# Kernel tuning notes

Hardware: AMD Instinct MI355X
Metric: run time of the kernel (lower is better)

## Reference

```python
import jax, jax.numpy as jnp
import numpy as np

N_NODES = 50000
N_EDGES = 800000


def _sage_conv(x, src, dst, Wl, Wr, b):
    # PyG SAGEConv (aggr='mean', root_weight=True):
    #   out_i = lin_l(mean_{j->i} x_j) + lin_r(x_i)
    msg = x[src]                                             # [E, F] gather
    agg = jax.ops.segment_sum(msg, dst, num_segments=N_NODES)
    deg = jax.ops.segment_sum(jnp.ones((msg.shape[0],), x.dtype), dst,
                              num_segments=N_NODES)
    agg = agg / jnp.maximum(deg, 1.0)[:, None]               # mean aggregation
    return agg @ Wl + x @ Wr + b


def setup_inputs() -> dict:
    key = jax.random.key(0)
    ks = jax.random.split(key, 9)
    Fin, H1, H2, Fout = 128, 256, 128, 64

    def w(k, fi, fo):
        return jax.random.normal(k, (fi, fo), jnp.float32) / np.sqrt(fi)

    return {
        "x": jax.random.normal(ks[0], (N_NODES, Fin), jnp.float32),
        "edge_index": jax.random.randint(ks[1], (2, N_EDGES), 0, N_NODES,
                                         dtype=jnp.int64),
        "Wl1": w(ks[2], Fin, H1), "Wr1": w(ks[3], Fin, H1),
        "b1": jnp.zeros((H1,), jnp.float32),
        "Wl2": w(ks[4], H1, H2), "Wr2": w(ks[5], H1, H2),
        "b2": jnp.zeros((H2,), jnp.float32),
        "Wl3": w(ks[6], H2, Fout), "Wr3": w(ks[7], H2, Fout),
        "b3": jnp.zeros((Fout,), jnp.float32),
    }


def reference(x, edge_index, Wl1, Wr1, b1, Wl2, Wr2, b2, Wl3, Wr3, b3):
    src, dst = edge_index[0], edge_index[1]
    # conv1 -> ReLU -> (dropout: identity in eval) -> conv2 -> ReLU -> conv3 -> Sigmoid
    h = jax.nn.relu(_sage_conv(x, src, dst, Wl1, Wr1, b1))
    h = jax.nn.relu(_sage_conv(h, src, dst, Wl2, Wr2, b2))
    out = jax.nn.sigmoid(_sage_conv(h, src, dst, Wl3, Wr3, b3))
    return out
```

## Files before the change

kernel.cpp:

```cpp
#include <hip/hip_runtime.h>
#include <cstddef>


using frag  = __attribute__((ext_vector_type(8))) short;
using f32x4 = __attribute__((ext_vector_type(4))) float;

constexpr int PBITS = 9;
constexpr int PSZ   = 1 << PBITS;
constexpr int PMAX  = 128;

__device__ __forceinline__ ushort f2bf(float f) {
    union { float f; unsigned u; } v; v.f = f;
    unsigned r = v.u + 0x7FFF + ((v.u >> 16) & 1);
    return (ushort)(r >> 16);
}
__device__ __forceinline__ float bf2f(ushort u) {
    union { unsigned u; float f; } v; v.u = ((unsigned)u) << 16;
    return v.f;
}


__global__ __launch_bounds__(256)
void k_pcount(const int* __restrict__ dst, int* __restrict__ pcount, int E, int P) {
    __shared__ int h[PMAX];
    int t = threadIdx.x;
    if (t < P) h[t] = 0;
    __syncthreads();
    int base = blockIdx.x * 4096;
    int n = min(4096, E - base);
    for (int i = t; i < n; i += 256)
        atomicAdd(&h[dst[base + i] >> PBITS], 1);
    __syncthreads();
    if (t < P && h[t]) atomicAdd(&pcount[t], h[t]);
}

__global__ void k_pscan(const int* __restrict__ pcount, int* __restrict__ pbase,
                        int* __restrict__ pcursor, int P) {
    if (threadIdx.x == 0) {
        int run = 0;
        for (int p = 0; p < P; ++p) { pbase[p] = run; pcursor[p] = run; run += pcount[p]; }
        pbase[P] = run;
    }
}

__global__ __launch_bounds__(256)
void k_scatter(const int* __restrict__ src, const int* __restrict__ dst,
               int* __restrict__ pcursor, unsigned* __restrict__ pairs, int E, int P) {
    __shared__ int h[PMAX];
    __shared__ int off[PMAX];
    int t = threadIdx.x;
    if (t < P) h[t] = 0;
    __syncthreads();
    int base = blockIdx.x * 4096;
    int pp[16]; int pr[16]; unsigned pk[16];
    #pragma unroll
    for (int ii = 0; ii < 16; ++ii) {
        int idx = base + ii * 256 + t;
        bool v = idx < E;
        int d = v ? dst[idx] : 0;
        int p = d >> PBITS;
        pp[ii] = v ? p : -1;
        pr[ii] = v ? atomicAdd(&h[p], 1) : 0;
        pk[ii] = v ? ((unsigned)src[idx] | ((unsigned)(d & (PSZ - 1)) << 16)) : 0u;
    }
    __syncthreads();
    if (t < P && h[t]) off[t] = atomicAdd(&pcursor[t], h[t]);
    __syncthreads();
    #pragma unroll
    for (int ii = 0; ii < 16; ++ii)
        if (pp[ii] >= 0) pairs[off[pp[ii]] + pr[ii]] = pk[ii];
}

__global__ __launch_bounds__(256)
void k_build(const unsigned* __restrict__ pairs, const int* __restrict__ pbase,
             int* __restrict__ deg, int* __restrict__ row_start,
             ushort* __restrict__ csr16, int M) {
    __shared__ int cnt[PSZ];
    __shared__ int ls[PSZ];
    __shared__ int fil[PSZ];
    __shared__ int ws[256];
    int pid = blockIdx.x;
    int t = threadIdx.x;
    int n0 = pid << PBITS;
    int L = min(PSZ, M - n0);
    int wb = pbase[pid], we = pbase[pid + 1];
    int ne = we - wb;
    for (int j = t; j < PSZ; j += 256) { cnt[j] = 0; fil[j] = 0; }
    __syncthreads();
    for (int i = t; i < ne; i += 256)
        atomicAdd(&cnt[pairs[wb + i] >> 16], 1);
    __syncthreads();
    int a = cnt[2 * t], b = cnt[2 * t + 1];
    ws[t] = a + b;
    __syncthreads();
    for (int o = 1; o < 256; o <<= 1) {
        int v = (t >= o) ? ws[t - o] : 0;
        __syncthreads();
        ws[t] += v;
        __syncthreads();
    }
    int excl = (t > 0) ? ws[t - 1] : 0;
    ls[2 * t] = excl; ls[2 * t + 1] = excl + a;
    __syncthreads();
    for (int j = t; j < L; j += 256) {
        deg[n0 + j] = cnt[j];
        row_start[n0 + j] = wb + ls[j];
    }
    for (int i = t; i < ne; i += 256) {
        unsigned pk = pairs[wb + i];
        int ln = pk >> 16;
        int pos = wb + ls[ln] + atomicAdd(&fil[ln], 1);
        csr16[pos] = (ushort)(pk & 0xFFFFu);
    }
}


__global__ void k_cvt_x(const float* __restrict__ in, ushort* __restrict__ out, int n4) {
    int i = blockIdx.x * blockDim.x + threadIdx.x;
    if (i < n4) {
        float4 v = ((const float4*)in)[i];
        ushort4 o; o.x = f2bf(v.x); o.y = f2bf(v.y); o.z = f2bf(v.z); o.w = f2bf(v.w);
        ((ushort4*)out)[i] = o;
    }
}

struct CvtDesc {
    const float* s[6];
    ushort*      d[6];
    int K[6];
    int N[6];
};

__global__ void k_cvt_w6(CvtDesc c) {
    int wi = blockIdx.y;
    int t = blockIdx.x * blockDim.x + threadIdx.x;
    int K = c.K[wi], N = c.N[wi];
    if (t < K * N) {
        int k = t / N, n = t % N;
        c.d[wi][(size_t)n * K + k] = f2bf(c.s[wi][t]);
    }
}


template <int F, int EPI>
__global__ __launch_bounds__(256)
void agg_bf(const ushort* __restrict__ in, const ushort* __restrict__ csr16,
            const int* __restrict__ row_start, const int* __restrict__ deg,
            const ushort* __restrict__ u, const float* __restrict__ bias,
            void* __restrict__ out, int nN) {
    constexpr int GPL = F / 4;
    constexpr int NPB = 256 / GPL;
    int gid  = threadIdx.x / GPL;
    int li   = threadIdx.x % GPL;
    int node = blockIdx.x * NPB + gid;
    bool valid = node < nN;
    int start = valid ? row_start[node] : 0;
    int d     = valid ? deg[node] : 0;
    float a0 = 0.f, a1 = 0.f, a2 = 0.f, a3 = 0.f;

    auto gat = [&](int j) {
        int s = csr16[start + j];
        ushort4 uv = *(const ushort4*)(in + (size_t)s * F + li * 4);
        a0 += bf2f(uv.x); a1 += bf2f(uv.y); a2 += bf2f(uv.z); a3 += bf2f(uv.w);
    };

    int j = 0;
    for (; j + 8 <= d; j += 8) {
        gat(j); gat(j+1); gat(j+2); gat(j+3);
        gat(j+4); gat(j+5); gat(j+6); gat(j+7);
    }
    for (; j + 2 <= d; j += 2) { gat(j); gat(j+1); }
    for (; j < d; ++j) gat(j);

    if (!valid) return;
    float inv = 1.f / (float)(d > 0 ? d : 1);
    a0 *= inv; a1 *= inv; a2 *= inv; a3 *= inv;

    size_t o4 = (size_t)node * F + li * 4;
    if constexpr (EPI == 0) {
        ushort4 o; o.x = f2bf(a0); o.y = f2bf(a1); o.z = f2bf(a2); o.w = f2bf(a3);
        *(ushort4*)((ushort*)out + o4) = o;
    } else {
        ushort4 uv = *(const ushort4*)(u + o4);
        float4 bv = *(const float4*)(bias + li * 4);
        a0 += bf2f(uv.x) + bv.x;
        a1 += bf2f(uv.y) + bv.y;
        a2 += bf2f(uv.z) + bv.z;
        a3 += bf2f(uv.w) + bv.w;
        if constexpr (EPI == 1) {
            ushort4 o;
            o.x = f2bf(fmaxf(a0, 0.f)); o.y = f2bf(fmaxf(a1, 0.f));
            o.z = f2bf(fmaxf(a2, 0.f)); o.w = f2bf(fmaxf(a3, 0.f));
            *(ushort4*)((ushort*)out + o4) = o;
        } else {
            float4 o;
            o.x = 1.f / (1.f + __expf(-a0)); o.y = 1.f / (1.f + __expf(-a1));
            o.z = 1.f / (1.f + __expf(-a2)); o.w = 1.f / (1.f + __expf(-a3));
            *(float4*)((float*)out + o4) = o;
        }
    }
}


__device__ __forceinline__ void gload16(const ushort* gp, char* lp) {
    __builtin_amdgcn_global_load_lds(
        (const __attribute__((address_space(1))) void*)gp,
        (__attribute__((address_space(3))) void*)lp, 16, 0, 0);
}

template <int BM, int BN, int WM, int WN, int ACT>
__global__ __launch_bounds__(WM * WN * 64)
void mgemm(const ushort* __restrict__ A1, const ushort* __restrict__ B1, int K1,
           const ushort* __restrict__ A2, const ushort* __restrict__ B2, int K2,
           const float* __restrict__ bias,
           ushort* __restrict__ C1, int ld1,
           ushort* __restrict__ C2, int ld2, int nsplit,
           int M, int N) {
    constexpr int NW = WM * WN;
    constexpr int MF = BM / (WM * 16);
    constexpr int NF = BN / (WN * 16);
    __shared__ char lds[(BM + BN) * 128];
    char* As = lds;
    char* Bs = lds + BM * 128;

    const int tid  = threadIdx.x;
    const int lane = tid & 63;
    const int wid  = tid >> 6;
    const int wm   = wid % WM, wn = wid / WM;
    const int bm   = blockIdx.x * BM;
    const int bn   = blockIdx.y * BN;
    const int l15  = lane & 15;
    const int lhi  = lane >> 4;
    const int lr8  = lane >> 3;
    const int lf   = lane & 7;

    f32x4 acc[MF][NF] = {};

    for (int pass = 0; pass < 2; ++pass) {
        const ushort* A = pass ? A2 : A1;
        const ushort* B = pass ? B2 : B1;
        const int K = pass ? K2 : K1;
        if (A == nullptr) continue;
        for (int k0 = 0; k0 < K; k0 += 64) {
            #pragma unroll
            for (int it = 0; it < BM / (8 * NW); ++it) {
                int r0 = (it * NW + wid) * 8;
                int row = r0 + lr8;
                int gr = bm + row; if (gr >= M) gr = M - 1;
                int gfc = lf ^ (row & 7);
                gload16(A + (size_t)gr * K + k0 + gfc * 8, As + r0 * 128);
            }
            #pragma unroll
            for (int it = 0; it < BN / (8 * NW); ++it) {
                int r0 = (it * NW + wid) * 8;
                int row = r0 + lr8;
                int gfc = lf ^ (row & 7);
                gload16(B + (size_t)(bn + row) * K + k0 + gfc * 8, Bs + r0 * 128);
            }
            __syncthreads();
            #pragma unroll
            for (int ks = 0; ks < 2; ++ks) {
                const int kb = ks * 64 + lhi * 16;
                frag a[MF], b[NF];
                #pragma unroll
                for (int mf = 0; mf < MF; ++mf) {
                    int row = wm * MF * 16 + mf * 16 + l15;
                    a[mf] = *(const frag*)(As + row * 128 + (kb ^ ((row & 7) << 4)));
                }
                #pragma unroll
                for (int nf = 0; nf < NF; ++nf) {
                    int row = wn * NF * 16 + nf * 16 + l15;
                    b[nf] = *(const frag*)(Bs + row * 128 + (kb ^ ((row & 7) << 4)));
                }
                #pragma unroll
                for (int mf = 0; mf < MF; ++mf)
                    #pragma unroll
                    for (int nf = 0; nf < NF; ++nf)
                        acc[mf][nf] = __builtin_amdgcn_mfma_f32_16x16x32_bf16(
                            a[mf], b[nf], acc[mf][nf], 0, 0, 0);
            }
            __syncthreads();
        }
    }

    #pragma unroll
    for (int mf = 0; mf < MF; ++mf) {
        #pragma unroll
        for (int r = 0; r < 4; ++r) {
            int gm = bm + wm * MF * 16 + mf * 16 + lhi * 4 + r;
            if (gm >= M) continue;
            #pragma unroll
            for (int nf = 0; nf < NF; ++nf) {
                int gn = bn + wn * NF * 16 + nf * 16 + l15;
                float v = acc[mf][nf][r];
                if (bias) v += bias[gn];
                if (ACT == 1) v = fmaxf(v, 0.f);
                ushort o = f2bf(v);
                if (gn < nsplit) C1[(size_t)gm * ld1 + gn] = o;
                else             C2[(size_t)gm * ld2 + (gn - nsplit)] = o;
            }
        }
    }
}


extern "C" void kernel_launch(void* const* d_in, const int* in_sizes, int n_in,
                              void* d_out, int out_size, void* d_ws, size_t ws_size,
                              hipStream_t stream) {
    const float* x   = (const float*)d_in[0];
    const int*   ei  = (const int*)d_in[1];
    const float* Wl1 = (const float*)d_in[2];
    const float* Wr1 = (const float*)d_in[3];
    const float* b1  = (const float*)d_in[4];
    const float* Wl2 = (const float*)d_in[5];
    const float* Wr2 = (const float*)d_in[6];
    const float* b2  = (const float*)d_in[7];
    const float* Wl3 = (const float*)d_in[8];
    const float* Wr3 = (const float*)d_in[9];
    const float* b3  = (const float*)d_in[10];

    const int M = in_sizes[0] / 128;
    const int E = in_sizes[1] / 2;
    const int P = (M + PSZ - 1) / PSZ;
    const int* src = ei;
    const int* dst = ei + E;

    char* w = (char*)d_ws;
    auto alloc = [&](size_t bytes) -> void* {
        void* p = (void*)w;
        w += (bytes + 255) & ~(size_t)255;
        return p;
    };
    int* pcount    = (int*)alloc((size_t)PMAX * 4);
    int* pbase     = (int*)alloc((size_t)(PMAX + 1) * 4);
    int* pcursor   = (int*)alloc((size_t)PMAX * 4);
    unsigned* pairs = (unsigned*)alloc((size_t)E * 4);
    ushort* csr16  = (ushort*)alloc((size_t)E * 2);
    int* deg       = (int*)alloc((size_t)M * 4);
    int* row_start = (int*)alloc((size_t)M * 4);
    ushort* Wl1t   = (ushort*)alloc(256 * 128 * 2);
    ushort* Wr1t   = (ushort*)alloc(256 * 128 * 2);
    ushort* Wcat2T = (ushort*)alloc(256 * 256 * 2);
    ushort* Wcat3T = (ushort*)alloc(128 * 128 * 2);
    ushort* bufA = (ushort*)alloc((size_t)M * 128 * 2);
    ushort* bufB = (ushort*)alloc((size_t)M * 128 * 2);
    ushort* bufH = (ushort*)alloc((size_t)M * 256 * 2);
    ushort* bufC = (ushort*)alloc((size_t)M * 128 * 2);
    (void)ws_size; (void)n_in; (void)out_size;

    ushort* x_bf = bufA; ushort* t2 = bufA; ushort* t3 = bufA;
    ushort* aggx = bufB; ushort* h2 = bufB;
    ushort* h1 = bufH;
    ushort* u2 = bufC;   ushort* u3 = bufC;

    hipMemsetAsync(pcount, 0, (size_t)PMAX * 4, stream);
    const int nchunk = (E + 4095) / 4096;
    k_pcount<<<nchunk, 256, 0, stream>>>(dst, pcount, E, P);
    k_pscan<<<1, 64, 0, stream>>>(pcount, pbase, pcursor, P);
    k_scatter<<<nchunk, 256, 0, stream>>>(src, dst, pcursor, pairs, E, P);
    k_build<<<P, 256, 0, stream>>>(pairs, pbase, deg, row_start, csr16, M);

    k_cvt_x<<<(M * 128 / 4 + 255) / 256, 256, 0, stream>>>(x, x_bf, M * 128 / 4);
    CvtDesc cd;
    cd.s[0] = Wl1; cd.d[0] = Wl1t;             cd.K[0] = 128; cd.N[0] = 256;
    cd.s[1] = Wr1; cd.d[1] = Wr1t;             cd.K[1] = 128; cd.N[1] = 256;
    cd.s[2] = Wl2; cd.d[2] = Wcat2T;           cd.K[2] = 256; cd.N[2] = 128;
    cd.s[3] = Wr2; cd.d[3] = Wcat2T + 128*256; cd.K[3] = 256; cd.N[3] = 128;
    cd.s[4] = Wl3; cd.d[4] = Wcat3T;           cd.K[4] = 128; cd.N[4] = 64;
    cd.s[5] = Wr3; cd.d[5] = Wcat3T + 64*128;  cd.K[5] = 128; cd.N[5] = 64;
    k_cvt_w6<<<dim3(128, 6), 256, 0, stream>>>(cd);

    const int gm128 = (M + 127) / 128;
    const int ga128 = (M + 7) / 8;
    const int ga64  = (M + 15) / 16;

    agg_bf<128, 0><<<ga128, 256, 0, stream>>>(x_bf, csr16, row_start, deg,
                                              nullptr, nullptr, aggx, M);
    mgemm<128, 64, 2, 2, 1><<<dim3(gm128, 4), 256, 0, stream>>>(
        aggx, Wl1t, 128, x_bf, Wr1t, 128, b1,
        h1, 256, nullptr, 0, 256, M, 256);

    mgemm<128, 64, 2, 2, 0><<<dim3(gm128, 4), 256, 0, stream>>>(
        h1, Wcat2T, 256, nullptr, nullptr, 0, nullptr,
        t2, 128, u2, 128, 128, M, 256);
    agg_bf<128, 1><<<ga128, 256, 0, stream>>>(t2, csr16, row_start, deg,
                                              u2, b2, h2, M);

    mgemm<128, 64, 2, 2, 0><<<dim3(gm128, 2), 256, 0, stream>>>(
        h2, Wcat3T, 128, nullptr, nullptr, 0, nullptr,
        t3, 64, u3, 64, 64, M, 128);
    agg_bf<64, 2><<<ga64, 256, 0, stream>>>(t3, csr16, row_start, deg,
                                            u3, b3, (float*)d_out, M);
}
```

Before: 215.7 us.

## Concatenate layer-1 operands, double-buffer GEMM LDS tiles, shrink GEMM tile to 64 rows

```diff
diff --git a/kernel.cpp b/kernel.cpp
--- a/kernel.cpp
+++ b/kernel.cpp
@@ -115,12 +115,14 @@
 }
 
 
-__global__ void k_cvt_x(const float* __restrict__ in, ushort* __restrict__ out, int n4) {
+__global__ void k_cvt_x(const float* __restrict__ in, ushort* __restrict__ AX, int n4) {
     int i = blockIdx.x * blockDim.x + threadIdx.x;
     if (i < n4) {
+        int row = i >> 5;
+        int c4  = i & 31;
         float4 v = ((const float4*)in)[i];
         ushort4 o; o.x = f2bf(v.x); o.y = f2bf(v.y); o.z = f2bf(v.z); o.w = f2bf(v.w);
-        ((ushort4*)out)[i] = o;
+        *(ushort4*)(AX + (size_t)row * 256 + 128 + c4 * 4) = o;
     }
 }
 
@@ -129,6 +131,8 @@
     ushort*      d[6];
     int K[6];
     int N[6];
+    int KD[6];
+    int KO[6];
 };
 
 __global__ void k_cvt_w6(CvtDesc c) {
@@ -137,12 +141,12 @@
     int K = c.K[wi], N = c.N[wi];
     if (t < K * N) {
         int k = t / N, n = t % N;
-        c.d[wi][(size_t)n * K + k] = f2bf(c.s[wi][t]);
-    }
-}
-
-
-template <int F, int EPI>
+        c.d[wi][(size_t)n * c.KD[wi] + c.KO[wi] + k] = f2bf(c.s[wi][t]);
+    }
+}
+
+
+template <int F, int EPI, int LDI, int LDO>
 __global__ __launch_bounds__(256)
 void agg_bf(const ushort* __restrict__ in, const ushort* __restrict__ csr16,
             const int* __restrict__ row_start, const int* __restrict__ deg,
@@ -160,7 +164,7 @@
 
     auto gat = [&](int j) {
         int s = csr16[start + j];
-        ushort4 uv = *(const ushort4*)(in + (size_t)s * F + li * 4);
+        ushort4 uv = *(const ushort4*)(in + (size_t)s * LDI + li * 4);
         a0 += bf2f(uv.x); a1 += bf2f(uv.y); a2 += bf2f(uv.z); a3 += bf2f(uv.w);
     };
 
@@ -176,12 +180,12 @@
     float inv = 1.f / (float)(d > 0 ? d : 1);
     a0 *= inv; a1 *= inv; a2 *= inv; a3 *= inv;
 
-    size_t o4 = (size_t)node * F + li * 4;
+    size_t o4 = (size_t)node * LDO + li * 4;
     if constexpr (EPI == 0) {
         ushort4 o; o.x = f2bf(a0); o.y = f2bf(a1); o.z = f2bf(a2); o.w = f2bf(a3);
         *(ushort4*)((ushort*)out + o4) = o;
     } else {
-        ushort4 uv = *(const ushort4*)(u + o4);
+        ushort4 uv = *(const ushort4*)(u + (size_t)node * F + li * 4);
         float4 bv = *(const float4*)(bias + li * 4);
         a0 += bf2f(uv.x) + bv.x;
         a1 += bf2f(uv.y) + bv.y;
@@ -208,20 +212,20 @@
         (__attribute__((address_space(3))) void*)lp, 16, 0, 0);
 }
 
-template <int BM, int BN, int WM, int WN, int ACT>
-__global__ __launch_bounds__(WM * WN * 64)
-void mgemm(const ushort* __restrict__ A1, const ushort* __restrict__ B1, int K1,
-           const ushort* __restrict__ A2, const ushort* __restrict__ B2, int K2,
+template <int BM, int BN, int K, int ACT>
+__global__ __launch_bounds__(256)
+void mgemm(const ushort* __restrict__ A, const ushort* __restrict__ B,
            const float* __restrict__ bias,
            ushort* __restrict__ C1, int ld1,
            ushort* __restrict__ C2, int ld2, int nsplit,
            int M, int N) {
-    constexpr int NW = WM * WN;
+    constexpr int NW = 4;
+    constexpr int WM = 2, WN = 2;
     constexpr int MF = BM / (WM * 16);
     constexpr int NF = BN / (WN * 16);
-    __shared__ char lds[(BM + BN) * 128];
-    char* As = lds;
-    char* Bs = lds + BM * 128;
+    constexpr int NSTEP = K / 64;
+    constexpr int TB = (BM + BN) * 128;
+    __shared__ char lds[2 * TB];
 
     const int tid  = threadIdx.x;
     const int lane = tid & 63;
@@ -234,52 +238,55 @@
     const int lr8  = lane >> 3;
     const int lf   = lane & 7;
 
+    auto stage = [&](int buf, int k0) {
+        char* As = lds + buf * TB;
+        char* Bs = As + BM * 128;
+        #pragma unroll
+        for (int it = 0; it < BM / (8 * NW); ++it) {
+            int r0 = (it * NW + wid) * 8;
+            int row = r0 + lr8;
+            int gr = bm + row; if (gr >= M) gr = M - 1;
+            int gfc = lf ^ (row & 7);
+            gload16(A + (size_t)gr * K + k0 + gfc * 8, As + r0 * 128);
+        }
+        #pragma unroll
+        for (int it = 0; it < BN / (8 * NW); ++it) {
+            int r0 = (it * NW + wid) * 8;
+            int row = r0 + lr8;
+            int gfc = lf ^ (row & 7);
+            gload16(B + (size_t)(bn + row) * K + k0 + gfc * 8, Bs + r0 * 128);
+        }
+    };
+
     f32x4 acc[MF][NF] = {};
 
-    for (int pass = 0; pass < 2; ++pass) {
-        const ushort* A = pass ? A2 : A1;
-        const ushort* B = pass ? B2 : B1;
-        const int K = pass ? K2 : K1;
-        if (A == nullptr) continue;
-        for (int k0 = 0; k0 < K; k0 += 64) {
+    stage(0, 0);
+    #pragma unroll
+    for (int s = 0; s < NSTEP; ++s) {
+        __syncthreads();
+        if (s + 1 < NSTEP) stage((s + 1) & 1, (s + 1) * 64);
+        char* As = lds + (s & 1) * TB;
+        char* Bs = As + BM * 128;
+        #pragma unroll
+        for (int ks = 0; ks < 2; ++ks) {
+            const int kb = ks * 64 + lhi * 16;
+            frag a[MF], b[NF];
             #pragma unroll
-            for (int it = 0; it < BM / (8 * NW); ++it) {
-                int r0 = (it * NW + wid) * 8;
-                int row = r0 + lr8;
-                int gr = bm + row; if (gr >= M) gr = M - 1;
-                int gfc = lf ^ (row & 7);
-                gload16(A + (size_t)gr * K + k0 + gfc * 8, As + r0 * 128);
+            for (int mf = 0; mf < MF; ++mf) {
+                int row = wm * MF * 16 + mf * 16 + l15;
+                a[mf] = *(const frag*)(As + row * 128 + (kb ^ ((row & 7) << 4)));
             }
             #pragma unroll
-            for (int it = 0; it < BN / (8 * NW); ++it) {
-                int r0 = (it * NW + wid) * 8;
-                int row = r0 + lr8;
-                int gfc = lf ^ (row & 7);
-                gload16(B + (size_t)(bn + row) * K + k0 + gfc * 8, Bs + r0 * 128);
+            for (int nf = 0; nf < NF; ++nf) {
+                int row = wn * NF * 16 + nf * 16 + l15;
+                b[nf] = *(const frag*)(Bs + row * 128 + (kb ^ ((row & 7) << 4)));
             }
-            __syncthreads();
             #pragma unroll
-            for (int ks = 0; ks < 2; ++ks) {
-                const int kb = ks * 64 + lhi * 16;
-                frag a[MF], b[NF];
+            for (int mf = 0; mf < MF; ++mf)
                 #pragma unroll
-                for (int mf = 0; mf < MF; ++mf) {
-                    int row = wm * MF * 16 + mf * 16 + l15;
-                    a[mf] = *(const frag*)(As + row * 128 + (kb ^ ((row & 7) << 4)));
-                }
-                #pragma unroll
-                for (int nf = 0; nf < NF; ++nf) {
-                    int row = wn * NF * 16 + nf * 16 + l15;
-                    b[nf] = *(const frag*)(Bs + row * 128 + (kb ^ ((row & 7) << 4)));
-                }
-                #pragma unroll
-                for (int mf = 0; mf < MF; ++mf)
-                    #pragma unroll
-                    for (int nf = 0; nf < NF; ++nf)
-                        acc[mf][nf] = __builtin_amdgcn_mfma_f32_16x16x32_bf16(
-                            a[mf], b[nf], acc[mf][nf], 0, 0, 0);
-            }
-            __syncthreads();
+                for (int nf = 0; nf < NF; ++nf)
+                    acc[mf][nf] = __builtin_amdgcn_mfma_f32_16x16x32_bf16(
+                        a[mf], b[nf], acc[mf][nf], 0, 0, 0);
         }
     }
 
@@ -338,18 +345,18 @@
     ushort* csr16  = (ushort*)alloc((size_t)E * 2);
     int* deg       = (int*)alloc((size_t)M * 4);
     int* row_start = (int*)alloc((size_t)M * 4);
-    ushort* Wl1t   = (ushort*)alloc(256 * 128 * 2);
-    ushort* Wr1t   = (ushort*)alloc(256 * 128 * 2);
+    ushort* Wcat1T = (ushort*)alloc(256 * 256 * 2);
     ushort* Wcat2T = (ushort*)alloc(256 * 256 * 2);
     ushort* Wcat3T = (ushort*)alloc(128 * 128 * 2);
+    ushort* AX   = (ushort*)alloc((size_t)M * 256 * 2);
     ushort* bufA = (ushort*)alloc((size_t)M * 128 * 2);
     ushort* bufB = (ushort*)alloc((size_t)M * 128 * 2);
     ushort* bufH = (ushort*)alloc((size_t)M * 256 * 2);
     ushort* bufC = (ushort*)alloc((size_t)M * 128 * 2);
     (void)ws_size; (void)n_in; (void)out_size;
 
-    ushort* x_bf = bufA; ushort* t2 = bufA; ushort* t3 = bufA;
-    ushort* aggx = bufB; ushort* h2 = bufB;
+    ushort* t2 = bufA; ushort* t3 = bufA;
+    ushort* h2 = bufB;
     ushort* h1 = bufH;
     ushort* u2 = bufC;   ushort* u3 = bufC;
 
@@ -360,35 +367,32 @@
     k_scatter<<<nchunk, 256, 0, stream>>>(src, dst, pcursor, pairs, E, P);
     k_build<<<P, 256, 0, stream>>>(pairs, pbase, deg, row_start, csr16, M);
 
-    k_cvt_x<<<(M * 128 / 4 + 255) / 256, 256, 0, stream>>>(x, x_bf, M * 128 / 4);
+    k_cvt_x<<<(M * 128 / 4 + 255) / 256, 256, 0, stream>>>(x, AX, M * 128 / 4);
     CvtDesc cd;
-    cd.s[0] = Wl1; cd.d[0] = Wl1t;             cd.K[0] = 128; cd.N[0] = 256;
-    cd.s[1] = Wr1; cd.d[1] = Wr1t;             cd.K[1] = 128; cd.N[1] = 256;
-    cd.s[2] = Wl2; cd.d[2] = Wcat2T;           cd.K[2] = 256; cd.N[2] = 128;
-    cd.s[3] = Wr2; cd.d[3] = Wcat2T + 128*256; cd.K[3] = 256; cd.N[3] = 128;
-    cd.s[4] = Wl3; cd.d[4] = Wcat3T;           cd.K[4] = 128; cd.N[4] = 64;
-    cd.s[5] = Wr3; cd.d[5] = Wcat3T + 64*128;  cd.K[5] = 128; cd.N[5] = 64;
+    cd.s[0] = Wl1; cd.d[0] = Wcat1T;           cd.K[0] = 128; cd.N[0] = 256; cd.KD[0] = 256; cd.KO[0] = 0;
+    cd.s[1] = Wr1; cd.d[1] = Wcat1T;           cd.K[1] = 128; cd.N[1] = 256; cd.KD[1] = 256; cd.KO[1] = 128;
+    cd.s[2] = Wl2; cd.d[2] = Wcat2T;           cd.K[2] = 256; cd.N[2] = 128; cd.KD[2] = 256; cd.KO[2] = 0;
+    cd.s[3] = Wr2; cd.d[3] = Wcat2T + 128*256; cd.K[3] = 256; cd.N[3] = 128; cd.KD[3] = 256; cd.KO[3] = 0;
+    cd.s[4] = Wl3; cd.d[4] = Wcat3T;           cd.K[4] = 128; cd.N[4] = 64;  cd.KD[4] = 128; cd.KO[4] = 0;
+    cd.s[5] = Wr3; cd.d[5] = Wcat3T + 64*128;  cd.K[5] = 128; cd.N[5] = 64;  cd.KD[5] = 128; cd.KO[5] = 0;
     k_cvt_w6<<<dim3(128, 6), 256, 0, stream>>>(cd);
 
-    const int gm128 = (M + 127) / 128;
+    const int gm64 = (M + 63) / 64;
     const int ga128 = (M + 7) / 8;
     const int ga64  = (M + 15) / 16;
 
-    agg_bf<128, 0><<<ga128, 256, 0, stream>>>(x_bf, csr16, row_start, deg,
-                                              nullptr, nullptr, aggx, M);
-    mgemm<128, 64, 2, 2, 1><<<dim3(gm128, 4), 256, 0, stream>>>(
-        aggx, Wl1t, 128, x_bf, Wr1t, 128, b1,
-        h1, 256, nullptr, 0, 256, M, 256);
-
-    mgemm<128, 64, 2, 2, 0><<<dim3(gm128, 4), 256, 0, stream>>>(
-        h1, Wcat2T, 256, nullptr, nullptr, 0, nullptr,
-        t2, 128, u2, 128, 128, M, 256);
-    agg_bf<128, 1><<<ga128, 256, 0, stream>>>(t2, csr16, row_start, deg,
-                                              u2, b2, h2, M);
-
-    mgemm<128, 64, 2, 2, 0><<<dim3(gm128, 2), 256, 0, stream>>>(
-        h2, Wcat3T, 128, nullptr, nullptr, 0, nullptr,
-        t3, 64, u3, 64, 64, M, 128);
-    agg_bf<64, 2><<<ga64, 256, 0, stream>>>(t3, csr16, row_start, deg,
-                                            u3, b3, (float*)d_out, M);
-}
+    agg_bf<128, 0, 256, 256><<<ga128, 256, 0, stream>>>(
+        AX + 128, csr16, row_start, deg, nullptr, nullptr, AX, M);
+    mgemm<64, 64, 256, 1><<<dim3(gm64, 4), 256, 0, stream>>>(
+        AX, Wcat1T, b1, h1, 256, h1, 256, 256, M, 256);
+
+    mgemm<64, 64, 256, 0><<<dim3(gm64, 4), 256, 0, stream>>>(
+        h1, Wcat2T, nullptr, t2, 128, u2, 128, 128, M, 256);
+    agg_bf<128, 1, 128, 128><<<ga128, 256, 0, stream>>>(
+        t2, csr16, row_start, deg, u2, b2, h2, M);
+
+    mgemm<64, 64, 128, 0><<<dim3(gm64, 2), 256, 0, stream>>>(
+        h2, Wcat3T, nullptr, t3, 64, u3, 64, 64, M, 128);
+    agg_bf<64, 2, 64, 64><<<ga64, 256, 0, stream>>>(
+        t3, csr16, row_start, deg, u3, b3, (float*)d_out, M);
+}
```

Result: faster. 211.1 us (median of 2 runs) (-2.1%).
